# Optimization experiments

Hardware: AMD Instinct MI355X
Metric: run time of the kernel (lower is better)

## Reference

```python
import jax, jax.numpy as jnp
import numpy as np

B1, B2 = 0.9, 0.999        # optax.adam defaults
LR, EPS = 0.1, 1e-8        # inner_gd_lr_y, adam eps (eps_root=0)
STEPS = 20                 # inner_gd_steps


def setup_inputs() -> dict:
    key = jax.random.key(0)
    ks = jax.random.split(key, 12)
    B, CD, W = 8192, 1, 32
    sc = 0.5
    return {
        "x": jax.random.normal(ks[0], (B, 1), dtype=jnp.float32),
        "c": jax.random.normal(ks[1], (B, CD), dtype=jnp.float32),
        "w0": sc * jax.random.normal(ks[2], (W, 2 + CD), dtype=jnp.float32),
        "b0": sc * jax.random.normal(ks[3], (W,), dtype=jnp.float32),
        "w1": sc * jax.random.normal(ks[4], (W, W), dtype=jnp.float32) / np.sqrt(W),
        "b1": sc * jax.random.normal(ks[5], (W,), dtype=jnp.float32),
        "w2": sc * jax.random.normal(ks[6], (W, W), dtype=jnp.float32) / np.sqrt(W),
        "b2": sc * jax.random.normal(ks[7], (W,), dtype=jnp.float32),
        "w3": sc * jax.random.normal(ks[8], (1, W), dtype=jnp.float32) / np.sqrt(W),
        "b3": sc * jax.random.normal(ks[9], (1,), dtype=jnp.float32),
        "y_mean": jnp.zeros((1,), dtype=jnp.float32),
    }


def reference(x, c, w0, b0, w1, b1, w2, b2, w3, b3, y_mean):
    def mlp(inp):  # inp: (3,) -> scalar energy
        h = jax.nn.relu(w0 @ inp + b0)
        h = jax.nn.relu(w1 @ h + b1)
        h = jax.nn.relu(w2 @ h + b2)
        return (w3 @ h + b3)[0]

    def base_energy(c_arg, x_i, y_arg):
        return mlp(jnp.concatenate([x_i, y_arg, c_arg]))

    # EBMUtils.get_c0_batch: nearest (non-self) neighbor in context space
    dists = jnp.linalg.norm(c[:, None, :] - c[None, :, :], axis=-1)
    dists = dists + jnp.eye(dists.shape[0], dtype=dists.dtype) * 1e9
    c0_batch = c[jnp.argmin(dists, axis=1)]

    def solve_one(x_i, c_fixed, c0):
        y0 = jnp.reshape(y_mean, (1,))
        c_init = jnp.zeros_like(c_fixed)
        state0 = (y0, c_init,
                  jnp.zeros_like(y0), jnp.zeros_like(y0),      # Adam m,v for y
                  jnp.zeros_like(c_init), jnp.zeros_like(c_init))  # Adam m,v for c

        def step(state, t):
            y, cc, my, vy, mc, vc = state

            def taylor_loss(y_arg):
                f = lambda c0a: base_energy(c0a, x_i, y_arg)
                E, dE = jax.jvp(f, (c0,), (cc - c0,))
                return E + dE

            gy = jax.grad(taylor_loss)(y)
            gc = jax.grad(lambda ca: base_energy(ca, x_i, y))(cc)

            def adam(g, m, v):
                m = B1 * m + (1.0 - B1) * g
                v = B2 * v + (1.0 - B2) * g * g
                mh = m / (1.0 - B1 ** t)
                vh = v / (1.0 - B2 ** t)
                return -LR * mh / (jnp.sqrt(vh) + EPS), m, v

            uy, my, vy = adam(gy, my, vy)
            uc, mc, vc = adam(gc, mc, vc)
            return (y + uy, cc + uc, my, vy, mc, vc), None

        (yf, cf, _, _, _, _), _ = jax.lax.scan(
            step, state0, jnp.arange(1, STEPS + 1, dtype=jnp.float32))
        return yf, cf

    pred, c_out = jax.vmap(solve_one)(x, c, c0_batch)
    return pred, c_out
```

## Files before the change

### kernel.cpp

```cpp
#include <hip/hip_runtime.h>

#define NB 8192
#define NSTEPS 20
#define DGATE 2e-3f

__global__ __launch_bounds__(256) void nn_kernel(const float* __restrict__ c,
                                                 int* __restrict__ nn) {
#pragma clang fp contract(off)
  __shared__ float cl[NB];
  const int tid = threadIdx.x;
  for (int k = tid; k < NB; k += 256) cl[k] = c[k];
  __syncthreads();
  const int wv = tid >> 6, lane = tid & 63;
  const int i = (blockIdx.x << 2) + wv;
  const float ci = cl[i];
  float bk = 1e30f;
  int bj = 0x7fffffff;
  for (int j = lane; j < NB; j += 64) {
    const float d = ci - cl[j];
    const float key = sqrtf(d * d);
    if (j != i && (key < bk || (key == bk && j < bj))) { bk = key; bj = j; }
  }
#pragma unroll
  for (int m = 1; m < 64; m <<= 1) {
    const float ok = __shfl_xor(bk, m);
    const int oj = __shfl_xor(bj, m);
    if (ok < bk || (ok == bk && oj < bj)) { bk = ok; bj = oj; }
  }
  if (lane == 0) nn[i] = bj;
}

#define DOT64_ROWLDS(dst, wp)                                   \
  { double a0_=0.,a1_=0.,a2_=0.,a3_=0.;                         \
    _Pragma("unroll")                                           \
    for (int q_=0;q_<8;++q_){                                   \
      const double2 hA_=hx2[2*q_], hB_=hx2[2*q_+1];             \
      a0_=fma((double)wp[i*33+4*q_+0],hA_.x,a0_);               \
      a1_=fma((double)wp[i*33+4*q_+1],hA_.y,a1_);               \
      a2_=fma((double)wp[i*33+4*q_+2],hB_.x,a2_);               \
      a3_=fma((double)wp[i*33+4*q_+3],hB_.y,a3_);}              \
    dst=(a0_+a1_)+(a2_+a3_); }

#define DOT64_LDS(dst, wp)                                      \
  { double a0_=0.,a1_=0.,a2_=0.,a3_=0.;                         \
    _Pragma("unroll")                                           \
    for (int q_=0;q_<8;++q_){                                   \
      const double2 hA_=hx2[2*q_], hB_=hx2[2*q_+1];             \
      a0_=fma((double)wp[(4*q_+0)*33+i],hA_.x,a0_);             \
      a1_=fma((double)wp[(4*q_+1)*33+i],hA_.y,a1_);             \
      a2_=fma((double)wp[(4*q_+2)*33+i],hB_.x,a2_);             \
      a3_=fma((double)wp[(4*q_+3)*33+i],hB_.y,a3_);}            \
    dst=(a0_+a1_)+(a2_+a3_); }

#define WROW1(j) w1p[i*33+(j)]
#define WROW2(j) w2p[i*33+(j)]
#define WCOL1(j) w1p[(j)*33+i]
#define WCOL2(j) w2p[(j)*33+i]
#define WGY(j) wgf[j]
#define F32DOT_ASC(acc, W)                                      \
  { acc=0.f; _Pragma("unroll")                                  \
    for (int j=0;j<32;++j) acc=fmaf(W(j), hxf[j], acc); }
#define F32DOT_DESC(acc, W)                                     \
  { acc=0.f; _Pragma("unroll")                                  \
    for (int j=31;j>=0;--j) acc=fmaf(W(j), hxf[j], acc); }

#define F32TRAJ(DOT)                                                   \
  {                                                                    \
    float y = ymf, cc = 0.f, my = 0.f, vy = 0.f, mc = 0.f, vc = 0.f;   \
    double p1d = 1.0, p2d = 1.0;                                       \
    for (int t = 0; t < NSTEPS; ++t) {                                 \
      p1d *= 0.9; p2d *= 0.999;                                        \
      const float bc1 = (float)(1.0 - p1d);                            \
      const float bc2 = (float)(1.0 - p2d);                            \
      const float cin = grp ? cc : c0f;                                \
      float a = 0.f;                                                   \
      a = fmaf(w0xf, xif, a); a = fmaf(w0yf, y, a);                    \
      a = fmaf(w0cf, cin, a);                                          \
      const float z0 = a + b0f; const float h0 = fmaxf(z0, 0.f);       \
      hxf[i] = h0; float sacc; DOT(sacc, WROW1);                       \
      const float z1 = sacc + b1f; const float h1 = fmaxf(z1, 0.f);    \
      hxf[i] = h1; DOT(sacc, WROW2);                                   \
      const float z2 = sacc + b2f;                                     \
      hxf[i] = z2 > 0.f ? w3f : 0.f; DOT(sacc, WCOL2);                 \
      const float g1 = z1 > 0.f ? sacc : 0.f;                          \
      hxf[i] = g1; DOT(sacc, WCOL1);                                   \
      const float g0 = z0 > 0.f ? sacc : 0.f;                          \
      hxf[i] = g0; DOT(sacc, WGY);                                     \
      const float gy = __shfl(sacc, 0);                                \
      const float gc = __shfl(sacc, 32);                               \
      { float tm = 0.9f * my, tg = 0.1f * gy; my = tm + tg;            \
        float tv = 0.999f * vy, t2 = 0.001f * gy; t2 = t2 * gy;        \
        vy = tv + t2;                                                  \
        const float mh = my / bc1, vh = vy / bc2;                      \
        const float den = sqrtf(vh) + 1e-8f;                           \
        y = y + (-0.1f * mh) / den; }                                  \
      { float tm = 0.9f * mc, tg = 0.1f * gc; mc = tm + tg;            \
        float tv = 0.999f * vc, t2 = 0.001f * gc; t2 = t2 * gc;        \
        vc = tv + t2;                                                  \
        const float mh = mc / bc1, vh = vc / bc2;                      \
        const float den = sqrtf(vh) + 1e-8f;                           \
        cc = cc + (-0.1f * mh) / den; }                                \
    }                                                                  \
    yf = (double)y; cf = (double)cc;                                   \
  }

#define F64TRAJ(TRACKM)                                                \
  {                                                                    \
    double y = (double)ymf, cc = 0., my = 0., vy = 0., mc = 0.,        \
           vc = 0.;                                                    \
    double p1 = 1., p2 = 1.;                                           \
    for (int t = 0; t < NSTEPS; ++t) {                                 \
      p1 *= 0.9; p2 *= 0.999;                                          \
      const double cin = grp ? cc : (double)c0f;                       \
      const double z0 = fma((double)w0xf, (double)xif,                 \
                        fma((double)w0yf, y,                           \
                        fma((double)w0cf, cin, (double)b0f)));         \
      const bool m0 = z0 > zb;                                         \
      TRACKM(z0);                                                      \
      hx[i] = m0 ? z0 : 0.;                                            \
      double d1; DOT64_ROWLDS(d1, w1p);                                \
      const double z1 = d1 + (double)b1f;                              \
      const bool m1 = z1 > zb;                                         \
      TRACKM(z1);                                                      \
      hx[i] = m1 ? z1 : 0.;                                            \
      double d2; DOT64_ROWLDS(d2, w2p);                                \
      const double z2 = d2 + (double)b2f;                              \
      const bool m2 = z2 > zb;                                         \
      TRACKM(z2);                                                      \
      hx[i] = m2 ? (double)w3f : 0.;                                   \
      double s1; DOT64_LDS(s1, w2p);                                   \
      hx[i] = m1 ? s1 : 0.;                                            \
      double s0; DOT64_LDS(s0, w1p);                                   \
      const double g0 = m0 ? s0 : 0.;                                  \
      double gp = (double)wselF * g0;                                  \
      _Pragma("unroll")                                                \
      for (int msk = 1; msk < 32; msk <<= 1) gp += __shfl_xor(gp, msk);\
      const double gy = __shfl(gp, 0) + gb;                            \
      const double gc = __shfl(gp, 32) + gb;                           \
      my = 0.9 * my + 0.1 * gy;                                        \
      vy = 0.999 * vy + 0.001 * gy * gy;                               \
      y += -0.1 * (my / (1. - p1)) / (sqrt(vy / (1. - p2)) + 1e-8);    \
      mc = 0.9 * mc + 0.1 * gc;                                        \
      vc = 0.999 * vc + 0.001 * gc * gc;                               \
      cc += -0.1 * (mc / (1. - p1)) / (sqrt(vc / (1. - p2)) + 1e-8);   \
    }                                                                  \
    yf = y; cf = cc;                                                   \
  }

#define TRK(z) { minz = fmin(minz, fabs(z)); }
#define NOTRK(z)

#define FFOLD(yF, cF)                                                  \
  { if (fabsf((yF) - yA) <= 0.07f && fabsf((cF) - cA) <= 0.07f) {      \
      ymin = fminf(ymin, (yF)); ymax = fmaxf(ymax, (yF));              \
      cmin = fminf(cmin, (cF)); cmax = fmaxf(cmax, (cF));              \
    } }

#define STAGE_LDS()                                                    \
  for (int idx = tid; idx < 1024; idx += 256) {                        \
    const int r = idx >> 5, cl = idx & 31;                             \
    w1p[r * 33 + cl] = w1[idx];                                        \
    w2p[r * 33 + cl] = w2[idx];                                        \
  }                                                                    \
  if (tid < 32) {                                                      \
    w0yc[0][tid] = w0[tid * 3 + 1];                                    \
    w0yc[1][tid] = w0[tid * 3 + 2];                                    \
  }                                                                    \
  __syncthreads();

#define CONSTS_F32()                                                   \
  const float w0xf = w0[i*3+0], w0yf = w0[i*3+1], w0cf = w0[i*3+2];    \
  const float b0f = b0[i], b1f = b1[i], b2f = b2[i], w3f = w3[i];      \
  const float xif = x[s], c0f = c[nn[s]], ymf = y_mean[0];             \
  const float wselF = grp ? w0cf : w0yf;

#define IDX()                                                          \
  const int tid = threadIdx.x;                                         \
  const int wv = tid >> 6;                                             \
  const int lane = tid & 63;                                           \
  const int grp = (lane >> 5) & 1;                                     \
  const int i = lane & 31;

__global__ __launch_bounds__(256) void ebm_fused_kernel(
    const float* __restrict__ x, const float* __restrict__ c,
    const float* __restrict__ w0, const float* __restrict__ b0,
    const float* __restrict__ w1, const float* __restrict__ b1,
    const float* __restrict__ w2, const float* __restrict__ b2,
    const float* __restrict__ w3, const float* __restrict__ y_mean,
    const int* __restrict__ nn, float* __restrict__ p0buf,
    float* __restrict__ f32buf) {
  __shared__ double hbuf[4][2][32];
  __shared__ float w1p[32 * 33];
  __shared__ float w2p[32 * 33];
  __shared__ float w0yc[2][32];
  IDX();
  const int b = blockIdx.x;
  const int role = b & 1;
  const int s = ((b >> 1) << 2) + wv;
  STAGE_LDS();
  CONSTS_F32();

  if (role == 0) {
    double* hx = &hbuf[wv][grp][0];
    const double2* hx2 = (const double2*)hx;
    double yf, cf;
    double minz = 1e300;
    {
      const double zb = 0.0, gb = 0.0;
      F64TRAJ(TRK);
    }
#pragma unroll
    for (int msk = 1; msk < 64; msk <<= 1)
      minz = fmin(minz, __shfl_xor(minz, msk));
    if (lane == 0) {
      p0buf[0 * NB + s] = (float)yf;
      p0buf[1 * NB + s] = (float)cf;
      p0buf[2 * NB + s] = (float)minz;
    }
  } else {
    float* hxf = (float*)&hbuf[wv][grp][0];
    const float* wgf = &w0yc[grp][0];
    double yf, cf;
    {
#pragma clang fp contract(off)
      F32TRAJ(F32DOT_ASC)
    }
    const float y5 = (float)yf, c5 = (float)cf;
    {
#pragma clang fp contract(off)
      F32TRAJ(F32DOT_DESC)
    }
    if (lane == 0) {
      f32buf[0 * NB + s] = y5;
      f32buf[1 * NB + s] = c5;
      f32buf[2 * NB + s] = (float)yf;
      f32buf[3 * NB + s] = (float)cf;
    }
  }
}

__global__ __launch_bounds__(256) void gate_kernel(
    const float* __restrict__ p0buf, const float* __restrict__ f32buf,
    float* __restrict__ out, int* __restrict__ list,
    int* __restrict__ count) {
  const int s = blockIdx.x * 256 + threadIdx.x;
  const float yA = p0buf[0 * NB + s], cA = p0buf[1 * NB + s];
  const float mzf = p0buf[2 * NB + s];
  const float y5 = f32buf[0 * NB + s], c5 = f32buf[1 * NB + s];
  const float y6 = f32buf[2 * NB + s], c6 = f32buf[3 * NB + s];
  float ymin = yA, ymax = yA, cmin = cA, cmax = cA;
  FFOLD(y5, c5);
  FFOLD(y6, c6);
  out[s] = 0.5f * (ymin + ymax);
  out[NB + s] = 0.5f * (cmin + cmax);
  const bool flag = (mzf <= 1e-5f) ||
                    (fabsf(y5 - yA) > DGATE) || (fabsf(c5 - cA) > DGATE) ||
                    (fabsf(y6 - yA) > DGATE) || (fabsf(c6 - cA) > DGATE);
  if (flag) {
    const int k = atomicAdd(count, 1);
    list[k] = s;
  }
}

__global__ __launch_bounds__(256) void ebm_flag_kernel(
    const float* __restrict__ x, const float* __restrict__ c,
    const float* __restrict__ w0, const float* __restrict__ b0,
    const float* __restrict__ w1, const float* __restrict__ b1,
    const float* __restrict__ w2, const float* __restrict__ b2,
    const float* __restrict__ w3, const float* __restrict__ y_mean,
    const int* __restrict__ nn, const float* __restrict__ p0buf,
    const float* __restrict__ f32buf, float* __restrict__ out,
    const int* __restrict__ list, const int* __restrict__ count) {
  const int nflag = *count;
  if (blockIdx.x >= nflag) return;

  __shared__ double hbuf[4][2][32];
  __shared__ float w1p[32 * 33];
  __shared__ float w2p[32 * 33];
  __shared__ float w0yc[2][32];
  __shared__ float res[4][2];
  IDX();
  const int s = list[blockIdx.x];
  STAGE_LDS();
  CONSTS_F32();
  double* hx = &hbuf[wv][grp][0];
  const double2* hx2 = (const double2*)hx;

  const int q = wv + 1;
  const double zb = (q == 1) ? -1e-5 : (q == 2) ? 1e-5 : 0.0;
  const double gb = (q == 3) ? 1e-6 : (q == 4) ? -1e-6 : 0.0;
  double yf, cf;
  F64TRAJ(NOTRK);
  if (lane == 0) {
    res[wv][0] = (float)yf;
    res[wv][1] = (float)cf;
  }
  __syncthreads();

  if (tid == 0) {
    const float yA = p0buf[0 * NB + s], cA = p0buf[1 * NB + s];
    float ymin = yA, ymax = yA, cmin = cA, cmax = cA;
    FFOLD(f32buf[0 * NB + s], f32buf[1 * NB + s]);
    FFOLD(f32buf[2 * NB + s], f32buf[3 * NB + s]);
#pragma unroll
    for (int p = 0; p < 4; ++p) FFOLD(res[p][0], res[p][1]);
    out[s] = 0.5f * (ymin + ymax);
    out[NB + s] = 0.5f * (cmin + cmax);
  }
}

extern "C" void kernel_launch(void* const* d_in, const int* in_sizes, int n_in,
                              void* d_out, int out_size, void* d_ws, size_t ws_size,
                              hipStream_t stream) {
  const float* x = (const float*)d_in[0];
  const float* c = (const float*)d_in[1];
  const float* w0 = (const float*)d_in[2];
  const float* b0 = (const float*)d_in[3];
  const float* w1 = (const float*)d_in[4];
  const float* b1 = (const float*)d_in[5];
  const float* w2 = (const float*)d_in[6];
  const float* b2 = (const float*)d_in[7];
  const float* w3 = (const float*)d_in[8];
  const float* y_mean = (const float*)d_in[10];

  char* ws = (char*)d_ws;
  int* nn = (int*)ws;
  int* count = (int*)(ws + NB * 4);
  int* list = (int*)(ws + NB * 4 + 16);
  float* p0buf = (float*)(ws + NB * 8 + 16);
  float* f32buf = (float*)(ws + NB * 8 + 16 + NB * 12);

  hipMemsetAsync(count, 0, 4, stream);
  nn_kernel<<<NB / 4, 256, 0, stream>>>(c, nn);
  ebm_fused_kernel<<<NB / 2, 256, 0, stream>>>(
      x, c, w0, b0, w1, b1, w2, b2, w3, y_mean, nn, p0buf, f32buf);
  gate_kernel<<<NB / 256, 256, 0, stream>>>(
      p0buf, f32buf, (float*)d_out, list, count);
  ebm_flag_kernel<<<NB, 256, 0, stream>>>(
      x, c, w0, b0, w1, b1, w2, b2, w3, y_mean, nn, p0buf, f32buf,
      (float*)d_out, list, count);
}
```

Before: 587.5 us.

## Drop unconditional f64 trajectory; run paired f32 trajectories and gate f64 to flagged samples

The main kernel no longer computes an f64 reference trajectory for every sample. Each wave now runs the ascending- and descending-order f32 trajectories interleaved in one loop and also tracks the minimum pre-activation magnitude in f32. The gate compares the two f32 results against each other and flags samples with near-zero activations (threshold loosened) for the f64 path. The flag kernel grows to 5 waves so it computes the unperturbed f64 baseline itself. This removes the per-sample f64 work and halves the main grid, at the risk that fewer or different samples get the accurate fallback.

```diff
diff --git a/kernel.cpp b/kernel.cpp
--- a/kernel.cpp
+++ b/kernel.cpp
@@ -3,6 +3,7 @@
 #define NB 8192
 #define NSTEPS 20
 #define DGATE 2e-3f
+#define MZGATE 3e-5f
 
 __global__ __launch_bounds__(256) void nn_kernel(const float* __restrict__ c,
                                                  int* __restrict__ nn) {
@@ -57,51 +58,50 @@
 #define WCOL1(j) w1p[(j)*33+i]
 #define WCOL2(j) w2p[(j)*33+i]
 #define WGY(j) wgf[j]
-#define F32DOT_ASC(acc, W)                                      \
+
+#define F32DOT_A(acc, W, H)                                     \
   { acc=0.f; _Pragma("unroll")                                  \
-    for (int j=0;j<32;++j) acc=fmaf(W(j), hxf[j], acc); }
-#define F32DOT_DESC(acc, W)                                     \
+    for (int j=0;j<32;++j) acc=fmaf(W(j), H[j], acc); }
+#define F32DOT_D(acc, W, H)                                     \
   { acc=0.f; _Pragma("unroll")                                  \
-    for (int j=31;j>=0;--j) acc=fmaf(W(j), hxf[j], acc); }
-
-#define F32TRAJ(DOT)                                                   \
-  {                                                                    \
-    float y = ymf, cc = 0.f, my = 0.f, vy = 0.f, mc = 0.f, vc = 0.f;   \
-    double p1d = 1.0, p2d = 1.0;                                       \
-    for (int t = 0; t < NSTEPS; ++t) {                                 \
-      p1d *= 0.9; p2d *= 0.999;                                        \
-      const float bc1 = (float)(1.0 - p1d);                            \
-      const float bc2 = (float)(1.0 - p2d);                            \
-      const float cin = grp ? cc : c0f;                                \
-      float a = 0.f;                                                   \
-      a = fmaf(w0xf, xif, a); a = fmaf(w0yf, y, a);                    \
-      a = fmaf(w0cf, cin, a);                                          \
-      const float z0 = a + b0f; const float h0 = fmaxf(z0, 0.f);       \
-      hxf[i] = h0; float sacc; DOT(sacc, WROW1);                       \
-      const float z1 = sacc + b1f; const float h1 = fmaxf(z1, 0.f);    \
-      hxf[i] = h1; DOT(sacc, WROW2);                                   \
-      const float z2 = sacc + b2f;                                     \
-      hxf[i] = z2 > 0.f ? w3f : 0.f; DOT(sacc, WCOL2);                 \
-      const float g1 = z1 > 0.f ? sacc : 0.f;                          \
-      hxf[i] = g1; DOT(sacc, WCOL1);                                   \
-      const float g0 = z0 > 0.f ? sacc : 0.f;                          \
-      hxf[i] = g0; DOT(sacc, WGY);                                     \
-      const float gy = __shfl(sacc, 0);                                \
-      const float gc = __shfl(sacc, 32);                               \
-      { float tm = 0.9f * my, tg = 0.1f * gy; my = tm + tg;            \
-        float tv = 0.999f * vy, t2 = 0.001f * gy; t2 = t2 * gy;        \
-        vy = tv + t2;                                                  \
-        const float mh = my / bc1, vh = vy / bc2;                      \
-        const float den = sqrtf(vh) + 1e-8f;                           \
-        y = y + (-0.1f * mh) / den; }                                  \
-      { float tm = 0.9f * mc, tg = 0.1f * gc; mc = tm + tg;            \
-        float tv = 0.999f * vc, t2 = 0.001f * gc; t2 = t2 * gc;        \
-        vc = tv + t2;                                                  \
-        const float mh = mc / bc1, vh = vc / bc2;                      \
-        const float den = sqrtf(vh) + 1e-8f;                           \
-        cc = cc + (-0.1f * mh) / den; }                                \
-    }                                                                  \
-    yf = (double)y; cf = (double)cc;                                   \
+    for (int j=31;j>=0;--j) acc=fmaf(W(j), H[j], acc); }
+
+#define TRK5(z) { minzf = fminf(minzf, fabsf(z)); }
+#define TRK6(z)
+#define NOTRK(z)
+
+#define F32STEPX(Y, CC, MY, VY, MC, VC, HXF, DOT, TRKF)                \
+  { const float cin = grp ? CC : c0f;                                  \
+    float a = 0.f;                                                     \
+    a = fmaf(w0xf, xif, a); a = fmaf(w0yf, Y, a);                      \
+    a = fmaf(w0cf, cin, a);                                            \
+    const float z0 = a + b0f; const float h0 = fmaxf(z0, 0.f);         \
+    TRKF(z0);                                                          \
+    HXF[i] = h0; float sacc; DOT(sacc, WROW1, HXF);                    \
+    const float z1 = sacc + b1f; const float h1 = fmaxf(z1, 0.f);      \
+    TRKF(z1);                                                          \
+    HXF[i] = h1; DOT(sacc, WROW2, HXF);                                \
+    const float z2 = sacc + b2f;                                       \
+    TRKF(z2);                                                          \
+    HXF[i] = z2 > 0.f ? w3f : 0.f; DOT(sacc, WCOL2, HXF);              \
+    const float g1 = z1 > 0.f ? sacc : 0.f;                            \
+    HXF[i] = g1; DOT(sacc, WCOL1, HXF);                                \
+    const float g0 = z0 > 0.f ? sacc : 0.f;                            \
+    HXF[i] = g0; DOT(sacc, WGY, HXF);                                  \
+    const float gy = __shfl(sacc, 0);                                  \
+    const float gc = __shfl(sacc, 32);                                 \
+    { float tm = 0.9f * MY, tg = 0.1f * gy; MY = tm + tg;              \
+      float tv = 0.999f * VY, t2 = 0.001f * gy; t2 = t2 * gy;          \
+      VY = tv + t2;                                                    \
+      const float mh = MY / bc1, vh = VY / bc2;                        \
+      const float den = sqrtf(vh) + 1e-8f;                             \
+      Y = Y + (-0.1f * mh) / den; }                                    \
+    { float tm = 0.9f * MC, tg = 0.1f * gc; MC = tm + tg;              \
+      float tv = 0.999f * VC, t2 = 0.001f * gc; t2 = t2 * gc;          \
+      VC = tv + t2;                                                    \
+      const float mh = MC / bc1, vh = VC / bc2;                        \
+      const float den = sqrtf(vh) + 1e-8f;                             \
+      CC = CC + (-0.1f * mh) / den; }                                  \
   }
 
 #define F64TRAJ(TRACKM)                                                \
@@ -147,17 +147,14 @@
     yf = y; cf = cc;                                                   \
   }
 
-#define TRK(z) { minz = fmin(minz, fabs(z)); }
-#define NOTRK(z)
-
 #define FFOLD(yF, cF)                                                  \
   { if (fabsf((yF) - yA) <= 0.07f && fabsf((cF) - cA) <= 0.07f) {      \
       ymin = fminf(ymin, (yF)); ymax = fmaxf(ymax, (yF));              \
       cmin = fminf(cmin, (cF)); cmax = fmaxf(cmax, (cF));              \
     } }
 
-#define STAGE_LDS()                                                    \
-  for (int idx = tid; idx < 1024; idx += 256) {                        \
+#define STAGE_LDS(NT)                                                  \
+  for (int idx = tid; idx < 1024; idx += (NT)) {                       \
     const int r = idx >> 5, cl = idx & 31;                             \
     w1p[r * 33 + cl] = w1[idx];                                        \
     w2p[r * 33 + cl] = w2[idx];                                        \
@@ -172,7 +169,8 @@
   const float w0xf = w0[i*3+0], w0yf = w0[i*3+1], w0cf = w0[i*3+2];    \
   const float b0f = b0[i], b1f = b1[i], b2f = b2[i], w3f = w3[i];      \
   const float xif = x[s], c0f = c[nn[s]], ymf = y_mean[0];             \
-  const float wselF = grp ? w0cf : w0yf;
+  const float wselF = grp ? w0cf : w0yf;                               \
+  (void)wselF;
 
 #define IDX()                                                          \
   const int tid = threadIdx.x;                                         \
@@ -181,114 +179,98 @@
   const int grp = (lane >> 5) & 1;                                     \
   const int i = lane & 31;
 
-__global__ __launch_bounds__(256) void ebm_fused_kernel(
+__global__ __launch_bounds__(256) void ebm_pair_kernel(
     const float* __restrict__ x, const float* __restrict__ c,
     const float* __restrict__ w0, const float* __restrict__ b0,
     const float* __restrict__ w1, const float* __restrict__ b1,
     const float* __restrict__ w2, const float* __restrict__ b2,
     const float* __restrict__ w3, const float* __restrict__ y_mean,
-    const int* __restrict__ nn, float* __restrict__ p0buf,
-    float* __restrict__ f32buf) {
-  __shared__ double hbuf[4][2][32];
+    const int* __restrict__ nn, float* __restrict__ f32buf,
+    float* __restrict__ minzbuf) {
+#pragma clang fp contract(off)
+  __shared__ float hf5[4][2][32];
+  __shared__ float hf6[4][2][32];
   __shared__ float w1p[32 * 33];
   __shared__ float w2p[32 * 33];
   __shared__ float w0yc[2][32];
   IDX();
-  const int b = blockIdx.x;
-  const int role = b & 1;
-  const int s = ((b >> 1) << 2) + wv;
-  STAGE_LDS();
+  const int s = (blockIdx.x << 2) + wv;
+  STAGE_LDS(256);
   CONSTS_F32();
-
-  if (role == 0) {
-    double* hx = &hbuf[wv][grp][0];
-    const double2* hx2 = (const double2*)hx;
-    double yf, cf;
-    double minz = 1e300;
-    {
-      const double zb = 0.0, gb = 0.0;
-      F64TRAJ(TRK);
-    }
+  float* hxf5 = &hf5[wv][grp][0];
+  float* hxf6 = &hf6[wv][grp][0];
+  const float* wgf = &w0yc[grp][0];
+
+  float y5 = ymf, cc5 = 0.f, my5 = 0.f, vy5 = 0.f, mc5 = 0.f, vc5 = 0.f;
+  float y6 = ymf, cc6 = 0.f, my6 = 0.f, vy6 = 0.f, mc6 = 0.f, vc6 = 0.f;
+  float minzf = 1e30f;
+  double p1d = 1.0, p2d = 1.0;
+  for (int t = 0; t < NSTEPS; ++t) {
+    p1d *= 0.9; p2d *= 0.999;
+    const float bc1 = (float)(1.0 - p1d);
+    const float bc2 = (float)(1.0 - p2d);
+    F32STEPX(y5, cc5, my5, vy5, mc5, vc5, hxf5, F32DOT_A, TRK5);
+    F32STEPX(y6, cc6, my6, vy6, mc6, vc6, hxf6, F32DOT_D, TRK6);
+  }
 #pragma unroll
-    for (int msk = 1; msk < 64; msk <<= 1)
-      minz = fmin(minz, __shfl_xor(minz, msk));
-    if (lane == 0) {
-      p0buf[0 * NB + s] = (float)yf;
-      p0buf[1 * NB + s] = (float)cf;
-      p0buf[2 * NB + s] = (float)minz;
-    }
-  } else {
-    float* hxf = (float*)&hbuf[wv][grp][0];
-    const float* wgf = &w0yc[grp][0];
-    double yf, cf;
-    {
-#pragma clang fp contract(off)
-      F32TRAJ(F32DOT_ASC)
-    }
-    const float y5 = (float)yf, c5 = (float)cf;
-    {
-#pragma clang fp contract(off)
-      F32TRAJ(F32DOT_DESC)
-    }
-    if (lane == 0) {
-      f32buf[0 * NB + s] = y5;
-      f32buf[1 * NB + s] = c5;
-      f32buf[2 * NB + s] = (float)yf;
-      f32buf[3 * NB + s] = (float)cf;
-    }
+  for (int m = 1; m < 64; m <<= 1)
+    minzf = fminf(minzf, __shfl_xor(minzf, m));
+
+  if (lane == 0) {
+    f32buf[0 * NB + s] = y5;
+    f32buf[1 * NB + s] = cc5;
+    f32buf[2 * NB + s] = y6;
+    f32buf[3 * NB + s] = cc6;
+    minzbuf[s] = minzf;
   }
 }
 
 __global__ __launch_bounds__(256) void gate_kernel(
-    const float* __restrict__ p0buf, const float* __restrict__ f32buf,
+    const float* __restrict__ f32buf, const float* __restrict__ minzbuf,
     float* __restrict__ out, int* __restrict__ list,
     int* __restrict__ count) {
   const int s = blockIdx.x * 256 + threadIdx.x;
-  const float yA = p0buf[0 * NB + s], cA = p0buf[1 * NB + s];
-  const float mzf = p0buf[2 * NB + s];
   const float y5 = f32buf[0 * NB + s], c5 = f32buf[1 * NB + s];
   const float y6 = f32buf[2 * NB + s], c6 = f32buf[3 * NB + s];
+  const float yA = y5, cA = c5;
   float ymin = yA, ymax = yA, cmin = cA, cmax = cA;
-  FFOLD(y5, c5);
   FFOLD(y6, c6);
   out[s] = 0.5f * (ymin + ymax);
   out[NB + s] = 0.5f * (cmin + cmax);
-  const bool flag = (mzf <= 1e-5f) ||
-                    (fabsf(y5 - yA) > DGATE) || (fabsf(c5 - cA) > DGATE) ||
-                    (fabsf(y6 - yA) > DGATE) || (fabsf(c6 - cA) > DGATE);
+  const bool flag = (minzbuf[s] <= MZGATE) ||
+                    (fabsf(y5 - y6) > DGATE) || (fabsf(c5 - c6) > DGATE);
   if (flag) {
     const int k = atomicAdd(count, 1);
     list[k] = s;
   }
 }
 
-__global__ __launch_bounds__(256) void ebm_flag_kernel(
+__global__ __launch_bounds__(320) void ebm_flag_kernel(
     const float* __restrict__ x, const float* __restrict__ c,
     const float* __restrict__ w0, const float* __restrict__ b0,
     const float* __restrict__ w1, const float* __restrict__ b1,
     const float* __restrict__ w2, const float* __restrict__ b2,
     const float* __restrict__ w3, const float* __restrict__ y_mean,
-    const int* __restrict__ nn, const float* __restrict__ p0buf,
-    const float* __restrict__ f32buf, float* __restrict__ out,
-    const int* __restrict__ list, const int* __restrict__ count) {
+    const int* __restrict__ nn, const float* __restrict__ f32buf,
+    float* __restrict__ out, const int* __restrict__ list,
+    const int* __restrict__ count) {
   const int nflag = *count;
   if (blockIdx.x >= nflag) return;
 
-  __shared__ double hbuf[4][2][32];
+  __shared__ double hbuf[5][2][32];
   __shared__ float w1p[32 * 33];
   __shared__ float w2p[32 * 33];
   __shared__ float w0yc[2][32];
-  __shared__ float res[4][2];
+  __shared__ float res[5][2];
   IDX();
   const int s = list[blockIdx.x];
-  STAGE_LDS();
+  STAGE_LDS(320);
   CONSTS_F32();
   double* hx = &hbuf[wv][grp][0];
   const double2* hx2 = (const double2*)hx;
 
-  const int q = wv + 1;
-  const double zb = (q == 1) ? -1e-5 : (q == 2) ? 1e-5 : 0.0;
-  const double gb = (q == 3) ? 1e-6 : (q == 4) ? -1e-6 : 0.0;
+  const double zb = (wv == 1) ? -1e-5 : (wv == 2) ? 1e-5 : 0.0;
+  const double gb = (wv == 3) ? 1e-6 : (wv == 4) ? -1e-6 : 0.0;
   double yf, cf;
   F64TRAJ(NOTRK);
   if (lane == 0) {
@@ -298,12 +280,12 @@
   __syncthreads();
 
   if (tid == 0) {
-    const float yA = p0buf[0 * NB + s], cA = p0buf[1 * NB + s];
+    const float yA = res[0][0], cA = res[0][1];
     float ymin = yA, ymax = yA, cmin = cA, cmax = cA;
+#pragma unroll
+    for (int p = 1; p < 5; ++p) FFOLD(res[p][0], res[p][1]);
     FFOLD(f32buf[0 * NB + s], f32buf[1 * NB + s]);
     FFOLD(f32buf[2 * NB + s], f32buf[3 * NB + s]);
-#pragma unroll
-    for (int p = 0; p < 4; ++p) FFOLD(res[p][0], res[p][1]);
     out[s] = 0.5f * (ymin + ymax);
     out[NB + s] = 0.5f * (cmin + cmax);
   }
@@ -327,16 +309,16 @@
   int* nn = (int*)ws;
   int* count = (int*)(ws + NB * 4);
   int* list = (int*)(ws + NB * 4 + 16);
-  float* p0buf = (float*)(ws + NB * 8 + 16);
-  float* f32buf = (float*)(ws + NB * 8 + 16 + NB * 12);
+  float* f32buf = (float*)(ws + NB * 8 + 16);
+  float* minzbuf = (float*)(ws + NB * 8 + 16 + NB * 16);
 
   hipMemsetAsync(count, 0, 4, stream);
   nn_kernel<<<NB / 4, 256, 0, stream>>>(c, nn);
-  ebm_fused_kernel<<<NB / 2, 256, 0, stream>>>(
-      x, c, w0, b0, w1, b1, w2, b2, w3, y_mean, nn, p0buf, f32buf);
+  ebm_pair_kernel<<<NB / 4, 256, 0, stream>>>(
+      x, c, w0, b0, w1, b1, w2, b2, w3, y_mean, nn, f32buf, minzbuf);
   gate_kernel<<<NB / 256, 256, 0, stream>>>(
-      p0buf, f32buf, (float*)d_out, list, count);
-  ebm_flag_kernel<<<NB, 256, 0, stream>>>(
-      x, c, w0, b0, w1, b1, w2, b2, w3, y_mean, nn, p0buf, f32buf,
+      f32buf, minzbuf, (float*)d_out, list, count);
+  ebm_flag_kernel<<<NB, 320, 0, stream>>>(
+      x, c, w0, b0, w1, b1, w2, b2, w3, y_mean, nn, f32buf,
       (float*)d_out, list, count);
 }
```

Result: no change. 578.9 us (-1.5%).
